# Optimization experiments

Hardware: AMD Instinct MI355X
Metric: run time of the kernel (lower is better)

Reference implementation:

```python
import jax, jax.numpy as jnp
import numpy as np

LEAKY_SLOPE = 0.2  # nn.LeakyReLU(alpha=0.2)


def setup_inputs() -> dict:
    key = jax.random.key(0)
    k1, k2, k3 = jax.random.split(key, 3)
    B, N, F_in = 8, 2048, 256
    H, D = 4, 64  # num_heads, out_per_head = out_features // num_heads
    h = jax.random.normal(k1, (B, N, F_in), dtype=jnp.float32)
    adj = jax.random.uniform(k2, (B, N, N), dtype=jnp.float32)
    # Linear(in_features, out_per_head, bias=False) per head, stacked: [H, F_in, D]
    W = jax.random.normal(k3, (H, F_in, D), dtype=jnp.float32) * (1.0 / np.sqrt(F_in))
    res_alpha = jnp.asarray(0.5, dtype=jnp.float32)  # ResidualWeight.alpha
    return {"h": h, "adj": adj, "W": W, "res_alpha": res_alpha}


def reference(h, adj, W, res_alpha):
    # adj passes through drop_edge (identity) and is otherwise unused.
    B, N, _ = h.shape
    H = W.shape[0]
    # h_prime per head: [H, B, N, D]
    hp = jnp.einsum("bnf,hfd->hbnd", h, W)
    # raw scores e[b,i,j] = <hp_i, hp_j>, then LeakyReLU, softmax over j (dim=2)
    e = jnp.einsum("hbnd,hbmd->hbnm", hp, hp)
    e = jnp.where(e >= 0, e, LEAKY_SLOPE * e)
    att = jax.nn.softmax(e, axis=-1)  # [H, B, N, N]
    # Faithful to source: output[b,i,d] = sum_j hp[b,i,d] * att[b,i,j]
    # (source broadcasts hp over j via unsqueeze(2).repeat, so index i is reused)
    out = hp * jnp.sum(att, axis=-1, keepdims=True)  # [H, B, N, D]
    # concat heads along feature dim -> [B, N, H*D]
    out = jnp.transpose(out, (1, 2, 0, 3)).reshape(B, N, -1)
    a = jnp.clip(res_alpha, 0.0, 1.0)
    return a * out + (1.0 - a) * h
```

## Files before the change

### kernel.cpp

```cpp
#include <hip/hip_runtime.h>
#include <hip/hip_bf16.h>


typedef unsigned short ushort_t;
typedef __bf16 bf16x8 __attribute__((ext_vector_type(8)));
typedef float floatx4 __attribute__((ext_vector_type(4)));

__device__ __forceinline__ ushort_t f2bf(float f) {
    unsigned int x;
    __builtin_memcpy(&x, &f, 4);
    return (ushort_t)((x + 0x7fffu + ((x >> 16) & 1u)) >> 16);
}

__global__ __launch_bounds__(256) void pack_w(const float* __restrict__ W,
                                              const float* __restrict__ alpha_p,
                                              ushort_t* __restrict__ Wb) {
    __shared__ float tile[64][68];
    const int h  = blockIdx.x >> 2;
    const int f0 = (blockIdx.x & 3) * 64;
    const int t  = threadIdx.x;

    float av = *alpha_p;
    av = fminf(fmaxf(av, 0.0f), 1.0f);
    const float bv = 1.0f - av;

    #pragma unroll
    for (int p = 0; p < 2; ++p) {
        const int fl = p * 32 + (t >> 3);
        const int d0 = (t & 7) * 8;
        const float* src = W + h * 16384 + (f0 + fl) * 64 + d0;
        *(float4*)&tile[fl][d0]     = *(const float4*)(src);
        *(float4*)&tile[fl][d0 + 4] = *(const float4*)(src + 4);
    }
    __syncthreads();

    #pragma unroll
    for (int p = 0; p < 2; ++p) {
        const int c    = p * 256 + t;
        const int kt2  = c >> 8;
        const int nt   = (c >> 6) & 3;
        const int lane = c & 63;
        const int kt   = (f0 >> 5) + kt2;
        const int d    = nt * 16 + (lane & 15);
        const int nglb = h * 64 + d;
        ushort_t tmp[8];
        #pragma unroll
        for (int j = 0; j < 8; ++j) {
            const int kglb = f0 + kt2 * 32 + ((lane >> 4) * 8) + j;
            float v = av * tile[kt2 * 32 + (lane >> 4) * 8 + j][d];
            if (kglb == nglb) v += bv;
            tmp[j] = f2bf(v);
        }
        *(uint4*)(Wb + (size_t)(((h * 8 + kt) * 4 + nt) * 64 + lane) * 8) =
            *(const uint4*)tmp;
    }
}

#define LDS_STRIDE 264

__global__ __launch_bounds__(256) void gat_gemm(const float* __restrict__ hIn,
                                                const ushort_t* __restrict__ Wb,
                                                float* __restrict__ out) {
    __shared__ ushort_t hA[32 * LDS_STRIDE];
    const int t  = threadIdx.x;
    const int m0 = blockIdx.x * 32;

    const int w    = t >> 6;
    const int lane = t & 63;
    const int quad = lane >> 4;
    const int l16  = lane & 15;

    const ushort_t* wbase = Wb + (size_t)w * 16384 + lane * 8;

    bf16x8 b[4];
    #pragma unroll
    for (int nt = 0; nt < 4; ++nt)
        b[nt] = *(const bf16x8*)(wbase + nt * 512);

    #pragma unroll
    for (int i = 0; i < 4; ++i) {
        const int c   = i * 256 + t;
        const int row = c >> 5;
        const int k8  = (c & 31) * 8;
        const float* src = hIn + (size_t)(m0 + row) * 256 + k8;
        float4 v0 = *(const float4*)(src);
        float4 v1 = *(const float4*)(src + 4);
        ushort_t tmp[8] = { f2bf(v0.x), f2bf(v0.y), f2bf(v0.z), f2bf(v0.w),
                            f2bf(v1.x), f2bf(v1.y), f2bf(v1.z), f2bf(v1.w) };
        *(uint4*)(hA + row * LDS_STRIDE + k8) = *(const uint4*)tmp;
    }
    __syncthreads();

    floatx4 acc[2][4] = {};

    #pragma unroll
    for (int kt = 0; kt < 8; ++kt) {
        bf16x8 bn[4];
        if (kt < 7) {
            #pragma unroll
            for (int nt = 0; nt < 4; ++nt)
                bn[nt] = *(const bf16x8*)(wbase + (kt + 1) * 2048 + nt * 512);
        }
        const int k0 = kt * 32 + quad * 8;
        bf16x8 a[2];
        #pragma unroll
        for (int mt = 0; mt < 2; ++mt)
            a[mt] = *(const bf16x8*)(hA + (mt * 16 + l16) * LDS_STRIDE + k0);
        #pragma unroll
        for (int mt = 0; mt < 2; ++mt)
            #pragma unroll
            for (int nt = 0; nt < 4; ++nt)
                acc[mt][nt] = __builtin_amdgcn_mfma_f32_16x16x32_bf16(
                    a[mt], b[nt], acc[mt][nt], 0, 0, 0);
        if (kt < 7) {
            #pragma unroll
            for (int nt = 0; nt < 4; ++nt) b[nt] = bn[nt];
        }
    }

    #pragma unroll
    for (int mt = 0; mt < 2; ++mt) {
        #pragma unroll
        for (int r = 0; r < 4; ++r) {
            const int rl = mt * 16 + quad * 4 + r;
            #pragma unroll
            for (int nt = 0; nt < 4; ++nt) {
                const int col = w * 64 + nt * 16 + l16;
                out[(size_t)(m0 + rl) * 256 + col] = acc[mt][nt][r];
            }
        }
    }
}

extern "C" void kernel_launch(void* const* d_in, const int* in_sizes, int n_in,
                              void* d_out, int out_size, void* d_ws, size_t ws_size,
                              hipStream_t stream) {
    const float* h_ptr = (const float*)d_in[0];
    const float* W_ptr = (const float*)d_in[2];
    const float* a_ptr = (const float*)d_in[3];
    float* out_ptr     = (float*)d_out;
    ushort_t* Wb       = (ushort_t*)d_ws;

    pack_w<<<16, 256, 0, stream>>>(W_ptr, a_ptr, Wb);
    gat_gemm<<<512, 256, 0, stream>>>(h_ptr, Wb, out_ptr);
}
```

Before: 182.4 us.

## Fuse weight packing into GEMM with per-head tiles and swizzled LDS

Removes the separate weight-pack kernel. Each block now converts its head's 256x64 weight slice to bf16 (folding in the residual alpha and identity) straight into swizzled LDS, alongside a 64-row tile of h. The grid is reorganised into 1024 blocks, one per 64-row by one-head tile, with a block-index remap and an XOR swizzle to avoid LDS bank conflicts. This saves a launch and the workspace round trip, but every block now redundantly reads and converts 64 KB of fp32 weights, and LDS use grows to 64 KB per block, which may reduce occupancy.

```diff
diff --git a/kernel.cpp b/kernel.cpp
--- a/kernel.cpp
+++ b/kernel.cpp
@@ -1,5 +1,4 @@
 #include <hip/hip_runtime.h>
-#include <hip/hip_bf16.h>
 
 
 typedef unsigned short ushort_t;
@@ -12,73 +11,50 @@
     return (ushort_t)((x + 0x7fffu + ((x >> 16) & 1u)) >> 16);
 }
 
-__global__ __launch_bounds__(256) void pack_w(const float* __restrict__ W,
-                                              const float* __restrict__ alpha_p,
-                                              ushort_t* __restrict__ Wb) {
-    __shared__ float tile[64][68];
-    const int h  = blockIdx.x >> 2;
-    const int f0 = (blockIdx.x & 3) * 64;
-    const int t  = threadIdx.x;
+#define TSTR 256
+
+__device__ __forceinline__ unsigned swz(int row, int kushort) {
+    unsigned byte = (unsigned)(row * TSTR + kushort) * 2u;
+    return byte ^ ((unsigned)(((row & 7) ^ (row >> 3)) & 7) << 4);
+}
+
+__global__ __launch_bounds__(256) void gat_fused(const float* __restrict__ hIn,
+                                                 const float* __restrict__ W,
+                                                 const float* __restrict__ alpha_p,
+                                                 float* __restrict__ out) {
+    __shared__ ushort_t Wt[64 * TSTR];
+    __shared__ ushort_t hA[64 * TSTR];
+    const int t = threadIdx.x;
+
+    const unsigned bid = blockIdx.x;
+    const unsigned wg  = ((bid & 7u) << 7) + (bid >> 3);
+    const int m0   = (int)(wg >> 2) * 64;
+    const int head = (int)(wg & 3u);
 
     float av = *alpha_p;
     av = fminf(fmaxf(av, 0.0f), 1.0f);
     const float bv = 1.0f - av;
 
     #pragma unroll
-    for (int p = 0; p < 2; ++p) {
-        const int fl = p * 32 + (t >> 3);
-        const int d0 = (t & 7) * 8;
-        const float* src = W + h * 16384 + (f0 + fl) * 64 + d0;
-        *(float4*)&tile[fl][d0]     = *(const float4*)(src);
-        *(float4*)&tile[fl][d0 + 4] = *(const float4*)(src + 4);
+    for (int i = 0; i < 8; ++i) {
+        const int c  = i * 256 + t;
+        const int k  = c >> 3;
+        const int d0 = (c & 7) * 8;
+        const float* src = W + head * 16384 + k * 64 + d0;
+        float4 v0 = *(const float4*)(src);
+        float4 v1 = *(const float4*)(src + 4);
+        float vv[8] = {v0.x, v0.y, v0.z, v0.w, v1.x, v1.y, v1.z, v1.w};
+        #pragma unroll
+        for (int j = 0; j < 8; ++j) {
+            const int d = d0 + j;
+            float v = av * vv[j];
+            if (k == head * 64 + d) v += bv;
+            *(ushort_t*)((char*)Wt + swz(d, k)) = f2bf(v);
+        }
     }
-    __syncthreads();
 
     #pragma unroll
-    for (int p = 0; p < 2; ++p) {
-        const int c    = p * 256 + t;
-        const int kt2  = c >> 8;
-        const int nt   = (c >> 6) & 3;
-        const int lane = c & 63;
-        const int kt   = (f0 >> 5) + kt2;
-        const int d    = nt * 16 + (lane & 15);
-        const int nglb = h * 64 + d;
-        ushort_t tmp[8];
-        #pragma unroll
-        for (int j = 0; j < 8; ++j) {
-            const int kglb = f0 + kt2 * 32 + ((lane >> 4) * 8) + j;
-            float v = av * tile[kt2 * 32 + (lane >> 4) * 8 + j][d];
-            if (kglb == nglb) v += bv;
-            tmp[j] = f2bf(v);
-        }
-        *(uint4*)(Wb + (size_t)(((h * 8 + kt) * 4 + nt) * 64 + lane) * 8) =
-            *(const uint4*)tmp;
-    }
-}
-
-#define LDS_STRIDE 264
-
-__global__ __launch_bounds__(256) void gat_gemm(const float* __restrict__ hIn,
-                                                const ushort_t* __restrict__ Wb,
-                                                float* __restrict__ out) {
-    __shared__ ushort_t hA[32 * LDS_STRIDE];
-    const int t  = threadIdx.x;
-    const int m0 = blockIdx.x * 32;
-
-    const int w    = t >> 6;
-    const int lane = t & 63;
-    const int quad = lane >> 4;
-    const int l16  = lane & 15;
-
-    const ushort_t* wbase = Wb + (size_t)w * 16384 + lane * 8;
-
-    bf16x8 b[4];
-    #pragma unroll
-    for (int nt = 0; nt < 4; ++nt)
-        b[nt] = *(const bf16x8*)(wbase + nt * 512);
-
-    #pragma unroll
-    for (int i = 0; i < 4; ++i) {
+    for (int i = 0; i < 8; ++i) {
         const int c   = i * 256 + t;
         const int row = c >> 5;
         const int k8  = (c & 31) * 8;
@@ -87,46 +63,46 @@
         float4 v1 = *(const float4*)(src + 4);
         ushort_t tmp[8] = { f2bf(v0.x), f2bf(v0.y), f2bf(v0.z), f2bf(v0.w),
                             f2bf(v1.x), f2bf(v1.y), f2bf(v1.z), f2bf(v1.w) };
-        *(uint4*)(hA + row * LDS_STRIDE + k8) = *(const uint4*)tmp;
+        *(uint4*)((char*)hA + swz(row, k8)) = *(const uint4*)tmp;
     }
     __syncthreads();
 
-    floatx4 acc[2][4] = {};
+    const int w    = t >> 6;
+    const int lane = t & 63;
+    const int quad = lane >> 4;
+    const int l16  = lane & 15;
+    const int ar0  = (w >> 1) * 32;
+    const int bc0  = (w & 1) * 32;
+
+    floatx4 acc[2][2] = {};
 
     #pragma unroll
     for (int kt = 0; kt < 8; ++kt) {
-        bf16x8 bn[4];
-        if (kt < 7) {
-            #pragma unroll
-            for (int nt = 0; nt < 4; ++nt)
-                bn[nt] = *(const bf16x8*)(wbase + (kt + 1) * 2048 + nt * 512);
-        }
         const int k0 = kt * 32 + quad * 8;
-        bf16x8 a[2];
+        bf16x8 a[2], b[2];
         #pragma unroll
         for (int mt = 0; mt < 2; ++mt)
-            a[mt] = *(const bf16x8*)(hA + (mt * 16 + l16) * LDS_STRIDE + k0);
+            a[mt] = *(const bf16x8*)((const char*)hA + swz(ar0 + mt * 16 + l16, k0));
+        #pragma unroll
+        for (int nt = 0; nt < 2; ++nt)
+            b[nt] = *(const bf16x8*)((const char*)Wt + swz(bc0 + nt * 16 + l16, k0));
         #pragma unroll
         for (int mt = 0; mt < 2; ++mt)
             #pragma unroll
-            for (int nt = 0; nt < 4; ++nt)
+            for (int nt = 0; nt < 2; ++nt)
                 acc[mt][nt] = __builtin_amdgcn_mfma_f32_16x16x32_bf16(
                     a[mt], b[nt], acc[mt][nt], 0, 0, 0);
-        if (kt < 7) {
-            #pragma unroll
-            for (int nt = 0; nt < 4; ++nt) b[nt] = bn[nt];
-        }
     }
 
     #pragma unroll
     for (int mt = 0; mt < 2; ++mt) {
         #pragma unroll
         for (int r = 0; r < 4; ++r) {
-            const int rl = mt * 16 + quad * 4 + r;
+            const int row = m0 + ar0 + mt * 16 + quad * 4 + r;
             #pragma unroll
-            for (int nt = 0; nt < 4; ++nt) {
-                const int col = w * 64 + nt * 16 + l16;
-                out[(size_t)(m0 + rl) * 256 + col] = acc[mt][nt][r];
+            for (int nt = 0; nt < 2; ++nt) {
+                const int col = head * 64 + bc0 + nt * 16 + l16;
+                out[(size_t)row * 256 + col] = acc[mt][nt][r];
             }
         }
     }
@@ -139,8 +115,6 @@
     const float* W_ptr = (const float*)d_in[2];
     const float* a_ptr = (const float*)d_in[3];
     float* out_ptr     = (float*)d_out;
-    ushort_t* Wb       = (ushort_t*)d_ws;
 
-    pack_w<<<16, 256, 0, stream>>>(W_ptr, a_ptr, Wb);
-    gat_gemm<<<512, 256, 0, stream>>>(h_ptr, Wb, out_ptr);
+    gat_fused<<<1024, 256, 0, stream>>>(h_ptr, W_ptr, a_ptr, out_ptr);
 }
```

After: 187.0 us. +2.5%, slower.
